# Kernel optimization log

Hardware: AMD Instinct MI355X
Metric: run time of the kernel (lower is better)

The kernel has to match this reference:

```python
import jax, jax.numpy as jnp
import numpy as np

H, B, D, C = 6, 512, 2048, 1000   # heads (5 ICs + backbone exit), batch, feat dim, classes
TAU = 0.5                          # confidence_threshold


def setup_inputs() -> dict:
    key = jax.random.key(0)
    k1, k2, k3, k4 = jax.random.split(key, 4)
    feats = jax.random.normal(k1, (H, B, D), dtype=jnp.float32)          # pooled reps at each exit
    W = jax.random.normal(k2, (H, D, C), dtype=jnp.float32) * 0.07       # per-head classifier weights
    b = jax.random.normal(k3, (H, C), dtype=jnp.float32) * 0.1
    y_true = jax.random.randint(k4, (B,), 0, C)
    return {"feats": feats, "W": W, "b": b, "y_true": y_true}


def reference(feats, W, b, y_true):
    # Per-head logits for every sample (vectorized replacement for the shrinking-batch loop).
    logits = jnp.einsum('hbd,hdc->hbc', feats, W) + b[:, None, :]        # [H, B, C]
    logp = jax.nn.log_softmax(logits, axis=-1)
    conf = jnp.exp(logp).max(axis=-1)                                    # [H, B] max softmax prob (prob_conf=True)

    # Early-exit routing: first head with conf >= TAU; else head with max confidence
    # (argmax returns the first occurrence, matching the strict '>' update in find_exit).
    exited = conf >= TAU                                                  # [H, B]
    any_exit = exited.any(axis=0)                                         # [B]
    first_exit = jnp.argmax(exited, axis=0)                               # [B] first True along heads
    best_conf = jnp.argmax(conf, axis=0)                                  # [B] fallback exit
    exit_idx = jnp.where(any_exit, first_exit, best_conf)                 # [B] == sample_exited_at

    # Gather the chosen head's logits per sample (vectorized masked-scatter of sample_outputs).
    outputs = jnp.take_along_axis(logits, exit_idx[None, :, None], axis=0)[0]   # [B, C]

    # criterion_ic: cross-entropy loss + accuracy on routed outputs
    out_logp = jax.nn.log_softmax(outputs, axis=-1)
    loss = -jnp.take_along_axis(out_logp, y_true[:, None], axis=1).mean()
    acc = (outputs.argmax(axis=-1) == y_true).astype(jnp.float32).mean()
    return outputs, exit_idx.astype(jnp.int32), loss, acc
```

## Files before the change

kernel.cpp:

```cpp
#include <hip/hip_runtime.h>
#include <hip/hip_bf16.h>
#include <math.h>

#define Hn 6
#define Bn 512
#define Dn 2048
#define Cn 1000
#define Cpad 1024
#define TAUv 0.5f
#define KSPLIT 2
#define KPER (Dn / KSPLIT)
#define NIT (KPER / 32)

typedef unsigned int u32;
typedef unsigned short u16;
typedef __attribute__((ext_vector_type(8))) short short8;
typedef __attribute__((ext_vector_type(4))) float f32x4;

union FragU { u32 d[4]; short8 s; };

__device__ __forceinline__ u32 cvt_pk2(float f0, float f1) {
  union { __hip_bfloat162 h; u32 u; } cv;
  cv.h = __float22bfloat162_rn(make_float2(f0, f1));
  return cv.u;
}

__device__ __forceinline__ void pack8f(const float* f, FragU& hi, FragU& lo) {
  float r[8];
#pragma unroll
  for (int i = 0; i < 4; ++i) {
    const u32 d = cvt_pk2(f[2 * i], f[2 * i + 1]);
    hi.d[i] = d;
    r[2 * i]     = f[2 * i]     - __uint_as_float(d << 16);
    r[2 * i + 1] = f[2 * i + 1] - __uint_as_float(d & 0xffff0000u);
  }
#pragma unroll
  for (int i = 0; i < 4; ++i) lo.d[i] = cvt_pk2(r[2 * i], r[2 * i + 1]);
}

__device__ __forceinline__ void dma16(const void* g, void* l) {
  __builtin_amdgcn_global_load_lds(
      (const __attribute__((address_space(1))) u32*)g,
      (__attribute__((address_space(3))) u32*)l, 16, 0, 0);
}

__global__ __launch_bounds__(256, 3) void gemm_k(
    const float* __restrict__ feats, const float* __restrict__ W,
    const float* __restrict__ bias, float* __restrict__ logits)
{
  const int h  = blockIdx.z >> 1;
  const int kz = blockIdx.z & 1;
  const int m0 = blockIdx.y * 128;
  const int n0 = blockIdx.x * 64;
  const int t = threadIdx.x, lane = t & 63, w = t >> 6;

  __shared__ __align__(16) float lds[2][6144];

  const int rA = (w & 1) * 64 + (lane >> 3);
  const int qA = (lane & 7) ^ ((lane >> 3) & 7);
  const float* gsrcA = feats + ((size_t)(h * Bn + m0 + rA)) * Dn + kz * KPER + qA * 4;
  const size_t gciA = (size_t)8 * Dn;
  const int dstA = w * 8192 + lane * 16;

  const int kb = (w - 2) * 16 + (lane >> 4);
  const int cB = lane & 15;
  const float* Wrow = W + ((size_t)h * Dn + kz * KPER) * Cn;
  const int dstB = 16384 + (w - 2) * 4096 + lane * 16;

  const int fl = lane & 15, fq = lane >> 4;
  const int wm = (w & 1) * 64, wn = (w >> 1) * 32;
  const int sxor = fl & 7;

  f32x4 acc[4][2];
#pragma unroll
  for (int i = 0; i < 4; ++i)
#pragma unroll
    for (int j = 0; j < 2; ++j) acc[i][j] = (f32x4){0.f, 0.f, 0.f, 0.f};

#define STAGE(TILE)                                                                   \
  {                                                                                   \
    char* sb = (char*)&lds[(TILE) & 1][0];                                            \
    if (w < 2) {                                                                      \
      const float* g = gsrcA + (size_t)(TILE) * 32;                                   \
      _Pragma("unroll")                                                               \
      for (int i = 0; i < 8; ++i) dma16(g + i * gciA, sb + dstA + i * 1024);          \
    } else {                                                                          \
      const size_t kt0 = (size_t)(TILE) * 32;                                         \
      _Pragma("unroll")                                                               \
      for (int i = 0; i < 4; ++i) {                                                   \
        const int kl = kb + 4 * i;                                                    \
        const int pc = cB ^ (((kl >> 3) & 1) << 2);                                   \
        int col = n0 + pc * 4;                                                        \
        col = (col + 3 < Cn) ? col : (Cn - 4);                                        \
        dma16(Wrow + (kt0 + kl) * Cn + col, sb + dstB + i * 1024);                    \
      }                                                                               \
    }                                                                                 \
  }

#define WAITCUR()                                                                     \
  {                                                                                   \
    if (w < 2) asm volatile("s_waitcnt vmcnt(8)" ::: "memory");                       \
    else       asm volatile("s_waitcnt vmcnt(4)" ::: "memory");                       \
  }

#define COMPUTE_TILE(IT)                                                              \
  {                                                                                   \
    const char*  ab = (const char*)&lds[(IT) & 1][0];                                 \
    const float* bb = (const float*)(ab + 16384);                                     \
    FragU ah[4], al[4];                                                               \
    _Pragma("unroll")                                                                 \
    for (int mt = 0; mt < 4; ++mt) {                                                  \
      const int r = wm + mt * 16 + fl;                                                \
      const float4 v0 = *(const float4*)(ab + r * 128 + ((((fq * 2)    ) ^ sxor) * 16)); \
      const float4 v1 = *(const float4*)(ab + r * 128 + ((((fq * 2) + 1) ^ sxor) * 16)); \
      float f[8] = {v0.x, v0.y, v0.z, v0.w, v1.x, v1.y, v1.z, v1.w};                  \
      pack8f(f, ah[mt], al[mt]);                                                      \
    }                                                                                 \
    _Pragma("unroll")                                                                 \
    for (int nt = 0; nt < 2; ++nt) {                                                  \
      const int n = wn + nt * 16 + fl;                                                \
      const int nsw = ((((n >> 2) ^ ((fq & 1) << 2)) << 2) | (n & 3));                \
      float f[8];                                                                     \
      _Pragma("unroll")                                                               \
      for (int e = 0; e < 8; ++e) f[e] = bb[(fq * 8 + e) * 64 + nsw];                 \
      FragU bh, bl;                                                                   \
      pack8f(f, bh, bl);                                                              \
      _Pragma("unroll")                                                               \
      for (int mt = 0; mt < 4; ++mt) {                                                \
        acc[mt][nt] = __builtin_amdgcn_mfma_f32_16x16x32_bf16(ah[mt].s, bh.s, acc[mt][nt], 0, 0, 0); \
        acc[mt][nt] = __builtin_amdgcn_mfma_f32_16x16x32_bf16(ah[mt].s, bl.s, acc[mt][nt], 0, 0, 0); \
        acc[mt][nt] = __builtin_amdgcn_mfma_f32_16x16x32_bf16(al[mt].s, bh.s, acc[mt][nt], 0, 0, 0); \
      }                                                                               \
    }                                                                                 \
  }

  STAGE(0);

  for (int it = 0; it < NIT - 1; ++it) {
    STAGE(it + 1);
    WAITCUR();
    __builtin_amdgcn_s_barrier();
    __builtin_amdgcn_sched_barrier(0);
    COMPUTE_TILE(it);
    __builtin_amdgcn_sched_barrier(0);
    asm volatile("s_waitcnt lgkmcnt(0)" ::: "memory");
    __builtin_amdgcn_s_barrier();
  }
  asm volatile("s_waitcnt vmcnt(0)" ::: "memory");
  __builtin_amdgcn_s_barrier();
  __builtin_amdgcn_sched_barrier(0);
  COMPUTE_TILE(NIT - 1);
#undef COMPUTE_TILE
#undef WAITCUR
#undef STAGE

  float* part = logits + (size_t)kz * ((size_t)Hn * Bn * Cn);
#pragma unroll
  for (int nt = 0; nt < 2; ++nt) {
    const int col = n0 + wn + nt * 16 + fl;
    if (col >= Cn) continue;
    const float bv = (kz == 0) ? bias[(size_t)h * Cn + col] : 0.f;
#pragma unroll
    for (int mt = 0; mt < 4; ++mt) {
      const int rbase = m0 + wm + mt * 16 + fq * 4;
#pragma unroll
      for (int r = 0; r < 4; ++r)
        part[((size_t)h * Bn + rbase + r) * Cn + col] = acc[mt][nt][r] + bv;
    }
  }
}

__global__ __launch_bounds__(256) void confpick_k(
    const float* __restrict__ logits, const int* __restrict__ y,
    float* __restrict__ out, float* __restrict__ out_exit,
    float* __restrict__ loss_b, float* __restrict__ corr_b)
{
  const int b = blockIdx.x, tid = threadIdx.x;
  const int lane = tid & 63, w = tid >> 6;
  const size_t S = (size_t)Hn * Bn * Cn;
  __shared__ float ms[Hn], ss[Hn];

  for (int h = w; h < Hn; h += 4) {
    const float* p = logits + ((size_t)h * Bn + b) * Cn;
    float vv[16];
#pragma unroll
    for (int i = 0; i < 4; ++i) {
      const int c4 = i * 256 + lane * 4;
      if (c4 + 3 < Cn) {
        const float4 v0 = *(const float4*)(p + c4);
        const float4 v1 = *(const float4*)(p + S + c4);
        vv[4 * i + 0] = v0.x + v1.x;
        vv[4 * i + 1] = v0.y + v1.y;
        vv[4 * i + 2] = v0.z + v1.z;
        vv[4 * i + 3] = v0.w + v1.w;
      } else {
#pragma unroll
        for (int j = 0; j < 4; ++j) {
          const int c = c4 + j;
          vv[4 * i + j] = (c < Cn) ? p[c] + p[S + c] : -3.4e38f;
        }
      }
    }
    float m = -3.4e38f;
#pragma unroll
    for (int i = 0; i < 16; ++i) m = fmaxf(m, vv[i]);
#pragma unroll
    for (int off = 32; off >= 1; off >>= 1) m = fmaxf(m, __shfl_xor(m, off));
    float s = 0.f;
#pragma unroll
    for (int i = 0; i < 16; ++i) s += (vv[i] > -3.0e38f) ? expf(vv[i] - m) : 0.f;
#pragma unroll
    for (int off = 32; off >= 1; off >>= 1) s += __shfl_xor(s, off);
    if (lane == 0) { ms[h] = m; ss[h] = s; }
  }
  __syncthreads();

  int first = -1, best = 0;
  float bestc = -3.4e38f;
#pragma unroll
  for (int h = 0; h < Hn; ++h) {
    const float c = 1.0f / ss[h];
    if (first < 0 && c >= TAUv) first = h;
    if (c > bestc) { bestc = c; best = h; }
  }
  const int ex = (first >= 0) ? first : best;
  const float* p = logits + ((size_t)ex * Bn + b) * Cn;

  const int c4 = tid * 4;
  float vv[4] = {-3.4e38f, -3.4e38f, -3.4e38f, -3.4e38f};
  if (c4 + 3 < Cn) {
    const float4 v0 = *(const float4*)(p + c4);
    const float4 v1 = *(const float4*)(p + S + c4);
    vv[0] = v0.x + v1.x;
    vv[1] = v0.y + v1.y;
    vv[2] = v0.z + v1.z;
    vv[3] = v0.w + v1.w;
  }
  float vm = -3.4e38f; int im = 1 << 30;
#pragma unroll
  for (int j = 0; j < 4; ++j) {
    const int c = c4 + j;
    if (c < Cn) {
      out[(size_t)b * Cn + c] = vv[j];
      if (vv[j] > vm) { vm = vv[j]; im = c; }
    }
  }
#pragma unroll
  for (int off = 32; off >= 1; off >>= 1) {
    const float ov = __shfl_xor(vm, off);
    const int   oi = __shfl_xor(im, off);
    if (ov > vm || (ov == vm && oi < im)) { vm = ov; im = oi; }
  }
  __shared__ float rm[4]; __shared__ int ri[4];
  if (lane == 0) { rm[w] = vm; ri[w] = im; }
  __syncthreads();
  if (tid == 0) {
    float bm = rm[0]; int bi = ri[0];
    for (int q = 1; q < 4; ++q)
      if (rm[q] > bm || (rm[q] == bm && ri[q] < bi)) { bm = rm[q]; bi = ri[q]; }
    const int yt = y[b];
    const float ryt = p[yt] + p[S + yt];
    const float lp = ryt - ms[ex] - logf(ss[ex]);
    out_exit[b] = (float)ex;
    loss_b[b] = -lp;
    corr_b[b] = (bi == yt) ? 1.f : 0.f;
  }
}

__global__ __launch_bounds__(256) void reduce_k(
    const float* __restrict__ loss_b, const float* __restrict__ corr_b,
    float* __restrict__ scalars)
{
  const int t = threadIdx.x, lane = t & 63, w = t >> 6;
  float l = loss_b[t] + loss_b[t + 256];
  float c = corr_b[t] + corr_b[t + 256];
#pragma unroll
  for (int off = 32; off >= 1; off >>= 1) {
    l += __shfl_xor(l, off);
    c += __shfl_xor(c, off);
  }
  __shared__ float sl[4], sc[4];
  if (lane == 0) { sl[w] = l; sc[w] = c; }
  __syncthreads();
  if (t == 0) {
    scalars[0] = (sl[0] + sl[1] + sl[2] + sl[3]) * (1.0f / (float)Bn);
    scalars[1] = (sc[0] + sc[1] + sc[2] + sc[3]) * (1.0f / (float)Bn);
  }
}

extern "C" void kernel_launch(void* const* d_in, const int* in_sizes, int n_in,
                              void* d_out, int out_size, void* d_ws, size_t ws_size,
                              hipStream_t stream) {
  const float* feats = (const float*)d_in[0];
  const float* W     = (const float*)d_in[1];
  const float* bias  = (const float*)d_in[2];
  const int*   y     = (const int*)d_in[3];
  float* out = (float*)d_out;

  float* logits = (float*)d_ws;
  float* loss_b = logits + (size_t)KSPLIT * Hn * Bn * Cn;
  float* corr_b = loss_b + Bn;
  float* out_exit    = out + (size_t)Bn * Cn;
  float* out_scalars = out + (size_t)Bn * Cn + Bn;

  gemm_k<<<dim3(Cpad / 64, Bn / 128, Hn * KSPLIT), 256, 0, stream>>>(
      feats, W, bias, logits);
  confpick_k<<<Bn, 256, 0, stream>>>(logits, y, out, out_exit, loss_b, corr_b);
  reduce_k<<<1, 256, 0, stream>>>(loss_b, corr_b, out_scalars);
}
```

Baseline: 181.7 us.

## Split softmax stats into per-row kernel, fuse final reduction via ticket, raise MFMA priority

The combined confidence/pick kernel is split in two. A stats kernel runs one 64-thread block per (head,batch) row, so all 3072 rows are reduced in parallel instead of 6 rows handled by 4 waves per block. The pick kernel reads those stats from global memory, and the separate reduce launch is folded into it with a last-block atomic ticket. The GEMM compute tile is also wrapped in s_setprio so MFMA waves get issue priority. Together these aim to raise parallelism in the epilogue and remove one launch, at the cost of an extra global round trip for the stats and an atomic.

```diff
diff --git a/kernel.cpp b/kernel.cpp
--- a/kernel.cpp
+++ b/kernel.cpp
@@ -141,7 +141,9 @@
     WAITCUR();
     __builtin_amdgcn_s_barrier();
     __builtin_amdgcn_sched_barrier(0);
+    __builtin_amdgcn_s_setprio(1);
     COMPUTE_TILE(it);
+    __builtin_amdgcn_s_setprio(0);
     __builtin_amdgcn_sched_barrier(0);
     asm volatile("s_waitcnt lgkmcnt(0)" ::: "memory");
     __builtin_amdgcn_s_barrier();
@@ -149,7 +151,9 @@
   asm volatile("s_waitcnt vmcnt(0)" ::: "memory");
   __builtin_amdgcn_s_barrier();
   __builtin_amdgcn_sched_barrier(0);
+  __builtin_amdgcn_s_setprio(1);
   COMPUTE_TILE(NIT - 1);
+  __builtin_amdgcn_s_setprio(0);
 #undef COMPUTE_TILE
 #undef WAITCUR
 #undef STAGE
@@ -170,56 +174,64 @@
   }
 }
 
-__global__ __launch_bounds__(256) void confpick_k(
-    const float* __restrict__ logits, const int* __restrict__ y,
+__global__ __launch_bounds__(64) void stats_k(
+    const float* __restrict__ logits, float* __restrict__ msA,
+    float* __restrict__ ssA, u32* __restrict__ ticket)
+{
+  const int id = blockIdx.x;
+  const int lane = threadIdx.x;
+  if (id == 0 && lane == 0) *ticket = 0;
+  const size_t S = (size_t)Hn * Bn * Cn;
+  const float* p = logits + (size_t)id * Cn;
+
+  float vv[16];
+#pragma unroll
+  for (int i = 0; i < 4; ++i) {
+    const int c4 = i * 256 + lane * 4;
+    if (c4 + 3 < Cn) {
+      const float4 v0 = *(const float4*)(p + c4);
+      const float4 v1 = *(const float4*)(p + S + c4);
+      vv[4 * i + 0] = v0.x + v1.x;
+      vv[4 * i + 1] = v0.y + v1.y;
+      vv[4 * i + 2] = v0.z + v1.z;
+      vv[4 * i + 3] = v0.w + v1.w;
+    } else {
+#pragma unroll
+      for (int j = 0; j < 4; ++j) {
+        const int c = c4 + j;
+        vv[4 * i + j] = (c < Cn) ? p[c] + p[S + c] : -3.4e38f;
+      }
+    }
+  }
+  float m = -3.4e38f;
+#pragma unroll
+  for (int i = 0; i < 16; ++i) m = fmaxf(m, vv[i]);
+#pragma unroll
+  for (int off = 32; off >= 1; off >>= 1) m = fmaxf(m, __shfl_xor(m, off));
+  float s = 0.f;
+#pragma unroll
+  for (int i = 0; i < 16; ++i) s += (vv[i] > -3.0e38f) ? expf(vv[i] - m) : 0.f;
+#pragma unroll
+  for (int off = 32; off >= 1; off >>= 1) s += __shfl_xor(s, off);
+  if (lane == 0) { msA[id] = m; ssA[id] = s; }
+}
+
+__global__ __launch_bounds__(256) void pick_k(
+    const float* __restrict__ logits, const float* __restrict__ msA,
+    const float* __restrict__ ssA, const int* __restrict__ y,
     float* __restrict__ out, float* __restrict__ out_exit,
-    float* __restrict__ loss_b, float* __restrict__ corr_b)
+    float* __restrict__ loss_b, float* __restrict__ corr_b,
+    u32* __restrict__ ticket, float* __restrict__ scalars)
 {
   const int b = blockIdx.x, tid = threadIdx.x;
   const int lane = tid & 63, w = tid >> 6;
   const size_t S = (size_t)Hn * Bn * Cn;
-  __shared__ float ms[Hn], ss[Hn];
-
-  for (int h = w; h < Hn; h += 4) {
-    const float* p = logits + ((size_t)h * Bn + b) * Cn;
-    float vv[16];
-#pragma unroll
-    for (int i = 0; i < 4; ++i) {
-      const int c4 = i * 256 + lane * 4;
-      if (c4 + 3 < Cn) {
-        const float4 v0 = *(const float4*)(p + c4);
-        const float4 v1 = *(const float4*)(p + S + c4);
-        vv[4 * i + 0] = v0.x + v1.x;
-        vv[4 * i + 1] = v0.y + v1.y;
-        vv[4 * i + 2] = v0.z + v1.z;
-        vv[4 * i + 3] = v0.w + v1.w;
-      } else {
-#pragma unroll
-        for (int j = 0; j < 4; ++j) {
-          const int c = c4 + j;
-          vv[4 * i + j] = (c < Cn) ? p[c] + p[S + c] : -3.4e38f;
-        }
-      }
-    }
-    float m = -3.4e38f;
-#pragma unroll
-    for (int i = 0; i < 16; ++i) m = fmaxf(m, vv[i]);
-#pragma unroll
-    for (int off = 32; off >= 1; off >>= 1) m = fmaxf(m, __shfl_xor(m, off));
-    float s = 0.f;
-#pragma unroll
-    for (int i = 0; i < 16; ++i) s += (vv[i] > -3.0e38f) ? expf(vv[i] - m) : 0.f;
-#pragma unroll
-    for (int off = 32; off >= 1; off >>= 1) s += __shfl_xor(s, off);
-    if (lane == 0) { ms[h] = m; ss[h] = s; }
-  }
-  __syncthreads();
 
   int first = -1, best = 0;
   float bestc = -3.4e38f;
 #pragma unroll
   for (int h = 0; h < Hn; ++h) {
-    const float c = 1.0f / ss[h];
+    const float c = 1.0f / ssA[h * Bn + b];
     if (first < 0 && c >= TAUv) first = h;
     if (c > bestc) { bestc = c; best = h; }
   }
@@ -252,6 +264,7 @@
     if (ov > vm || (ov == vm && oi < im)) { vm = ov; im = oi; }
   }
   __shared__ float rm[4]; __shared__ int ri[4];
+  __shared__ u32 tk;
   if (lane == 0) { rm[w] = vm; ri[w] = im; }
   __syncthreads();
   if (tid == 0) {
@@ -260,31 +273,31 @@
       if (rm[q] > bm || (rm[q] == bm && ri[q] < bi)) { bm = rm[q]; bi = ri[q]; }
     const int yt = y[b];
     const float ryt = p[yt] + p[S + yt];
-    const float lp = ryt - ms[ex] - logf(ss[ex]);
+    const float lp = ryt - msA[ex * Bn + b] - logf(ssA[ex * Bn + b]);
     out_exit[b] = (float)ex;
     loss_b[b] = -lp;
     corr_b[b] = (bi == yt) ? 1.f : 0.f;
-  }
-}
-
-__global__ __launch_bounds__(256) void reduce_k(
-    const float* __restrict__ loss_b, const float* __restrict__ corr_b,
-    float* __restrict__ scalars)
-{
-  const int t = threadIdx.x, lane = t & 63, w = t >> 6;
-  float l = loss_b[t] + loss_b[t + 256];
-  float c = corr_b[t] + corr_b[t + 256];
-#pragma unroll
-  for (int off = 32; off >= 1; off >>= 1) {
-    l += __shfl_xor(l, off);
-    c += __shfl_xor(c, off);
-  }
-  __shared__ float sl[4], sc[4];
-  if (lane == 0) { sl[w] = l; sc[w] = c; }
+    __threadfence();
+    tk = atomicAdd(ticket, 1u);
+  }
   __syncthreads();
-  if (t == 0) {
-    scalars[0] = (sl[0] + sl[1] + sl[2] + sl[3]) * (1.0f / (float)Bn);
-    scalars[1] = (sc[0] + sc[1] + sc[2] + sc[3]) * (1.0f / (float)Bn);
+
+  if (tk == (u32)(Bn - 1)) {
+    __threadfence();
+    float l = loss_b[tid] + loss_b[tid + 256];
+    float c = corr_b[tid] + corr_b[tid + 256];
+#pragma unroll
+    for (int off = 32; off >= 1; off >>= 1) {
+      l += __shfl_xor(l, off);
+      c += __shfl_xor(c, off);
+    }
+    __shared__ float sl[4], sc[4];
+    if (lane == 0) { sl[w] = l; sc[w] = c; }
+    __syncthreads();
+    if (tid == 0) {
+      scalars[0] = (sl[0] + sl[1] + sl[2] + sl[3]) * (1.0f / (float)Bn);
+      scalars[1] = (sc[0] + sc[1] + sc[2] + sc[3]) * (1.0f / (float)Bn);
+    }
   }
 }
 
@@ -300,11 +313,15 @@
   float* logits = (float*)d_ws;
   float* loss_b = logits + (size_t)KSPLIT * Hn * Bn * Cn;
   float* corr_b = loss_b + Bn;
+  float* msA    = corr_b + Bn;
+  float* ssA    = msA + Hn * Bn;
+  u32*   ticket = (u32*)(ssA + Hn * Bn);
   float* out_exit    = out + (size_t)Bn * Cn;
   float* out_scalars = out + (size_t)Bn * Cn + Bn;
 
   gemm_k<<<dim3(Cpad / 64, Bn / 128, Hn * KSPLIT), 256, 0, stream>>>(
       feats, W, bias, logits);
-  confpick_k<<<Bn, 256, 0, stream>>>(logits, y, out, out_exit, loss_b, corr_b);
-  reduce_k<<<1, 256, 0, stream>>>(loss_b, corr_b, out_scalars);
-}
+  stats_k<<<Hn * Bn, 64, 0, stream>>>(logits, msA, ssA, ticket);
+  pick_k<<<Bn, 256, 0, stream>>>(logits, msA, ssA, y, out, out_exit,
+                                 loss_b, corr_b, ticket, out_scalars);
+}
```

New measurement: 186.7 us. +2.8%, slower.

## Pre-split fp32 operands into bf16 hi/lo fragment layout in a separate pass

Applied to the files above, without the earlier changes.

Adds a conversion kernel that splits feats and W into bf16 hi/lo pairs, stored in an MFMA-fragment-friendly layout. The GEMM then loads those fragments straight from LDS, so the per-tile fp32-to-bf16 packing disappears from the inner loop. The GEMM tile is widened to 128x128, blocks are remapped for locality, and s_setprio is raised around the compute section. The cost is an extra launch plus writing and re-reading the converted operands through global memory, and occupancy drops to 2 blocks.

```diff
diff --git a/kernel.cpp b/kernel.cpp
--- a/kernel.cpp
+++ b/kernel.cpp
@@ -11,6 +11,7 @@
 #define KSPLIT 2
 #define KPER (Dn / KSPLIT)
 #define NIT (KPER / 32)
+#define NKT (Dn / 32)
 
 typedef unsigned int u32;
 typedef unsigned short u16;
@@ -25,17 +26,20 @@
   return cv.u;
 }
 
-__device__ __forceinline__ void pack8f(const float* f, FragU& hi, FragU& lo) {
+__device__ __forceinline__ void pack8(const float* rr, uint4& hv, uint4& lv) {
+  u32 hd[4], ld[4];
   float r[8];
 #pragma unroll
   for (int i = 0; i < 4; ++i) {
-    const u32 d = cvt_pk2(f[2 * i], f[2 * i + 1]);
-    hi.d[i] = d;
-    r[2 * i]     = f[2 * i]     - __uint_as_float(d << 16);
-    r[2 * i + 1] = f[2 * i + 1] - __uint_as_float(d & 0xffff0000u);
-  }
-#pragma unroll
-  for (int i = 0; i < 4; ++i) lo.d[i] = cvt_pk2(r[2 * i], r[2 * i + 1]);
+    const u32 d = cvt_pk2(rr[2 * i], rr[2 * i + 1]);
+    hd[i] = d;
+    r[2 * i]     = rr[2 * i]     - __uint_as_float(d << 16);
+    r[2 * i + 1] = rr[2 * i + 1] - __uint_as_float(d & 0xffff0000u);
+  }
+#pragma unroll
+  for (int i = 0; i < 4; ++i) ld[i] = cvt_pk2(r[2 * i], r[2 * i + 1]);
+  hv = make_uint4(hd[0], hd[1], hd[2], hd[3]);
+  lv = make_uint4(ld[0], ld[1], ld[2], ld[3]);
 }
 
 __device__ __forceinline__ void dma16(const void* g, void* l) {
@@ -44,87 +48,135 @@
       (__attribute__((address_space(3))) u32*)l, 16, 0, 0);
 }
 
-__global__ __launch_bounds__(256, 3) void gemm_k(
+__global__ __launch_bounds__(256) void conv_k(
     const float* __restrict__ feats, const float* __restrict__ W,
+    u16* __restrict__ Ah, u16* __restrict__ Al,
+    u16* __restrict__ Bh, u16* __restrict__ Bl)
+{
+  __shared__ float smem[128 * 33];
+  const int t   = blockIdx.x;
+  const int yy  = blockIdx.y;
+  const int h   = blockIdx.z;
+  const int tid = threadIdx.x;
+
+  if (yy < 4) {
+    const int r0 = yy * 128;
+#pragma unroll
+    for (int i = 0; i < 4; ++i) {
+      const int f = i * 256 + tid;
+      const int r = f >> 3, q = f & 7;
+      const float4 v = *(const float4*)(feats + ((size_t)(h * Bn + r0 + r) * Dn + t * 32 + q * 4));
+      smem[r * 33 + q * 4 + 0] = v.x; smem[r * 33 + q * 4 + 1] = v.y;
+      smem[r * 33 + q * 4 + 2] = v.z; smem[r * 33 + q * 4 + 3] = v.w;
+    }
+    __syncthreads();
+#pragma unroll
+    for (int i = 0; i < 2; ++i) {
+      const int j = i * 256 + tid;
+      const int c = j >> 7, r = j & 127;
+      float rr[8];
+#pragma unroll
+      for (int e = 0; e < 8; ++e) rr[e] = smem[r * 33 + c * 8 + e];
+      uint4 hv, lv;
+      pack8(rr, hv, lv);
+      const size_t o = (((size_t)(h * 64 + t) * 4 + c) * 512 + r0 + r);
+      ((uint4*)Ah)[o] = hv;
+      ((uint4*)Al)[o] = lv;
+    }
+  } else {
+    const int n0 = (yy - 4) * 128;
+#pragma unroll
+    for (int i = 0; i < 4; ++i) {
+      const int f = i * 256 + tid;
+      const int k = f >> 5, q = f & 31;
+      const int n = n0 + q * 4;
+      const float* src = W + ((size_t)h * Dn + t * 32 + k) * Cn;
+      float4 v = make_float4(0.f, 0.f, 0.f, 0.f);
+      if (n + 3 < Cn) {
+        v = *(const float4*)(src + n);
+      } else {
+        if (n + 0 < Cn) v.x = src[n + 0];
+        if (n + 1 < Cn) v.y = src[n + 1];
+        if (n + 2 < Cn) v.z = src[n + 2];
+        if (n + 3 < Cn) v.w = src[n + 3];
+      }
+      smem[k * 129 + q * 4 + 0] = v.x; smem[k * 129 + q * 4 + 1] = v.y;
+      smem[k * 129 + q * 4 + 2] = v.z; smem[k * 129 + q * 4 + 3] = v.w;
+    }
+    __syncthreads();
+#pragma unroll
+    for (int i = 0; i < 2; ++i) {
+      const int j = i * 256 + tid;
+      const int c = j >> 7, n = j & 127;
+      float rr[8];
+#pragma unroll
+      for (int e = 0; e < 8; ++e) rr[e] = smem[(c * 8 + e) * 129 + n];
+      uint4 hv, lv;
+      pack8(rr, hv, lv);
+      const size_t o = (((size_t)(h * 64 + t) * 4 + c) * 1024 + n0 + n);
+      ((uint4*)Bh)[o] = hv;
+      ((uint4*)Bl)[o] = lv;
+    }
+  }
+}
+
+__global__ __launch_bounds__(256, 2) void gemm_k(
+    const u16* __restrict__ AhG, const u16* __restrict__ AlG,
+    const u16* __restrict__ BhG, const u16* __restrict__ BlG,
     const float* __restrict__ bias, float* __restrict__ logits)
 {
-  const int h  = blockIdx.z >> 1;
-  const int kz = blockIdx.z & 1;
-  const int m0 = blockIdx.y * 128;
-  const int n0 = blockIdx.x * 64;
+  const int bid = blockIdx.x;
+  const int wg = (bid & 7) * 48 + (bid >> 3);
+  const int n0 = (wg & 7) * 128;
+  const int m0 = ((wg >> 3) & 3) * 128;
+  const int z  = wg >> 5;
+  const int h  = z >> 1;
+  const int kz = z & 1;
   const int t = threadIdx.x, lane = t & 63, w = t >> 6;
 
-  __shared__ __align__(16) float lds[2][6144];
-
-  const int rA = (w & 1) * 64 + (lane >> 3);
-  const int qA = (lane & 7) ^ ((lane >> 3) & 7);
-  const float* gsrcA = feats + ((size_t)(h * Bn + m0 + rA)) * Dn + kz * KPER + qA * 4;
-  const size_t gciA = (size_t)8 * Dn;
-  const int dstA = w * 8192 + lane * 16;
-
-  const int kb = (w - 2) * 16 + (lane >> 4);
-  const int cB = lane & 15;
-  const float* Wrow = W + ((size_t)h * Dn + kz * KPER) * Cn;
-  const int dstB = 16384 + (w - 2) * 4096 + lane * 16;
+  __shared__ __align__(16) char lds[2][32768];
+
+  const u16* gmat = (w == 0) ? AhG : (w == 1) ? AlG : (w == 2) ? BhG : BlG;
+  const int  R    = (w < 2) ? 512 : 1024;
+  const int  row0 = (w < 2) ? m0 : n0;
+  const uint4* g0 = (const uint4*)gmat
+                  + ((size_t)(h * 64 + kz * NIT) * 4) * R + row0 + lane;
+  const int dstw = w * 8192 + lane * 16;
 
   const int fl = lane & 15, fq = lane >> 4;
-  const int wm = (w & 1) * 64, wn = (w >> 1) * 32;
-  const int sxor = fl & 7;
-
-  f32x4 acc[4][2];
+  const int wm = (w & 1) * 64, wn = (w >> 1) * 64;
+
+  f32x4 acc[4][4];
 #pragma unroll
   for (int i = 0; i < 4; ++i)
 #pragma unroll
-    for (int j = 0; j < 2; ++j) acc[i][j] = (f32x4){0.f, 0.f, 0.f, 0.f};
+    for (int j = 0; j < 4; ++j) acc[i][j] = (f32x4){0.f, 0.f, 0.f, 0.f};
 
 #define STAGE(TILE)                                                                   \
   {                                                                                   \
-    char* sb = (char*)&lds[(TILE) & 1][0];                                            \
-    if (w < 2) {                                                                      \
-      const float* g = gsrcA + (size_t)(TILE) * 32;                                   \
-      _Pragma("unroll")                                                               \
-      for (int i = 0; i < 8; ++i) dma16(g + i * gciA, sb + dstA + i * 1024);          \
-    } else {                                                                          \
-      const size_t kt0 = (size_t)(TILE) * 32;                                         \
-      _Pragma("unroll")                                                               \
-      for (int i = 0; i < 4; ++i) {                                                   \
-        const int kl = kb + 4 * i;                                                    \
-        const int pc = cB ^ (((kl >> 3) & 1) << 2);                                   \
-        int col = n0 + pc * 4;                                                        \
-        col = (col + 3 < Cn) ? col : (Cn - 4);                                        \
-        dma16(Wrow + (kt0 + kl) * Cn + col, sb + dstB + i * 1024);                    \
-      }                                                                               \
-    }                                                                                 \
-  }
-
-#define WAITCUR()                                                                     \
-  {                                                                                   \
-    if (w < 2) asm volatile("s_waitcnt vmcnt(8)" ::: "memory");                       \
-    else       asm volatile("s_waitcnt vmcnt(4)" ::: "memory");                       \
+    char* sb = &lds[(TILE) & 1][0];                                                   \
+    const uint4* g = g0 + (size_t)(TILE) * 4 * R;                                     \
+    _Pragma("unroll")                                                                 \
+    for (int i = 0; i < 8; ++i)                                                       \
+      dma16(g + (size_t)(i >> 1) * R + (i & 1) * 64, sb + dstw + i * 1024);           \
   }
 
 #define COMPUTE_TILE(IT)                                                              \
   {                                                                                   \
-    const char*  ab = (const char*)&lds[(IT) & 1][0];                                 \
-    const float* bb = (const float*)(ab + 16384);                                     \
+    const char* bb = &lds[(IT) & 1][0];                                               \
     FragU ah[4], al[4];                                                               \
     _Pragma("unroll")                                                                 \
     for (int mt = 0; mt < 4; ++mt) {                                                  \
       const int r = wm + mt * 16 + fl;                                                \
-      const float4 v0 = *(const float4*)(ab + r * 128 + ((((fq * 2)    ) ^ sxor) * 16)); \
-      const float4 v1 = *(const float4*)(ab + r * 128 + ((((fq * 2) + 1) ^ sxor) * 16)); \
-      float f[8] = {v0.x, v0.y, v0.z, v0.w, v1.x, v1.y, v1.z, v1.w};                  \
-      pack8f(f, ah[mt], al[mt]);                                                      \
+      ah[mt].s = *(const short8*)(bb + (fq * 128 + r) * 16);                          \
+      al[mt].s = *(const short8*)(bb + 8192 + (fq * 128 + r) * 16);                   \
     }                                                                                 \
     _Pragma("unroll")                                                                 \
-    for (int nt = 0; nt < 2; ++nt) {                                                  \
+    for (int nt = 0; nt < 4; ++nt) {                                                  \
       const int n = wn + nt * 16 + fl;                                                \
-      const int nsw = ((((n >> 2) ^ ((fq & 1) << 2)) << 2) | (n & 3));                \
-      float f[8];                                                                     \
-      _Pragma("unroll")                                                               \
-      for (int e = 0; e < 8; ++e) f[e] = bb[(fq * 8 + e) * 64 + nsw];                 \
       FragU bh, bl;                                                                   \
-      pack8f(f, bh, bl);                                                              \
+      bh.s = *(const short8*)(bb + 16384 + (fq * 128 + n) * 16);                      \
+      bl.s = *(const short8*)(bb + 24576 + (fq * 128 + n) * 16);                      \
       _Pragma("unroll")                                                               \
       for (int mt = 0; mt < 4; ++mt) {                                                \
         acc[mt][nt] = __builtin_amdgcn_mfma_f32_16x16x32_bf16(ah[mt].s, bh.s, acc[mt][nt], 0, 0, 0); \
@@ -138,10 +190,12 @@
 
   for (int it = 0; it < NIT - 1; ++it) {
     STAGE(it + 1);
-    WAITCUR();
+    asm volatile("s_waitcnt vmcnt(8)" ::: "memory");
     __builtin_amdgcn_s_barrier();
     __builtin_amdgcn_sched_barrier(0);
+    __builtin_amdgcn_s_setprio(1);
     COMPUTE_TILE(it);
+    __builtin_amdgcn_s_setprio(0);
     __builtin_amdgcn_sched_barrier(0);
     asm volatile("s_waitcnt lgkmcnt(0)" ::: "memory");
     __builtin_amdgcn_s_barrier();
@@ -149,14 +203,15 @@
   asm volatile("s_waitcnt vmcnt(0)" ::: "memory");
   __builtin_amdgcn_s_barrier();
   __builtin_amdgcn_sched_barrier(0);
+  __builtin_amdgcn_s_setprio(1);
   COMPUTE_TILE(NIT - 1);
+  __builtin_amdgcn_s_setprio(0);
 #undef COMPUTE_TILE
-#undef WAITCUR
 #undef STAGE
 
   float* part = logits + (size_t)kz * ((size_t)Hn * Bn * Cn);
 #pragma unroll
-  for (int nt = 0; nt < 2; ++nt) {
+  for (int nt = 0; nt < 4; ++nt) {
     const int col = n0 + wn + nt * 16 + fl;
     if (col >= Cn) continue;
     const float bv = (kz == 0) ? bias[(size_t)h * Cn + col] : 0.f;
@@ -300,11 +355,15 @@
   float* logits = (float*)d_ws;
   float* loss_b = logits + (size_t)KSPLIT * Hn * Bn * Cn;
   float* corr_b = loss_b + Bn;
+  u16*   AhG    = (u16*)(corr_b + Bn + 64);
+  u16*   AlG    = AhG + (size_t)Hn * NKT * 4 * 512 * 8;
+  u16*   BhG    = AlG + (size_t)Hn * NKT * 4 * 512 * 8;
+  u16*   BlG    = BhG + (size_t)Hn * NKT * 4 * 1024 * 8;
   float* out_exit    = out + (size_t)Bn * Cn;
   float* out_scalars = out + (size_t)Bn * Cn + Bn;
 
-  gemm_k<<<dim3(Cpad / 64, Bn / 128, Hn * KSPLIT), 256, 0, stream>>>(
-      feats, W, bias, logits);
+  conv_k<<<dim3(NKT, 12, Hn), 256, 0, stream>>>(feats, W, AhG, AlG, BhG, BlG);
+  gemm_k<<<dim3(384, 1, 1), 256, 0, stream>>>(AhG, AlG, BhG, BlG, bias, logits);
   confpick_k<<<Bn, 256, 0, stream>>>(logits, y, out, out_exit, loss_b, corr_b);
   reduce_k<<<1, 256, 0, stream>>>(loss_b, corr_b, out_scalars);
 }
```

Result: faster. 169.8 us (-6.6%).
